# Kernel optimization log

Measured on AMD Instinct MI355X. Metric: run time of the kernel, lower is better.

## Reference

```python
import jax, jax.numpy as jnp
import numpy as np

DIM = 96; NH = 3; HD = DIM // NH; SCALE = HD ** -0.5
WS = (7, 7, 7); N = WS[0] * WS[1] * WS[2]
SHIFT = (3, 3, 3)  # half window
NL = 2
GRID = (28, 28, 28)
B = 2


def _rel_index():
    wd, wh, ww = WS
    coords = np.stack(np.meshgrid(np.arange(wd), np.arange(wh), np.arange(ww), indexing='ij')).reshape(3, -1)
    rel = (coords[:, :, None] - coords[:, None, :]).transpose(1, 2, 0)  # [N,N,3]
    rel[..., 0] += wd - 1; rel[..., 1] += wh - 1; rel[..., 2] += ww - 1
    rel[..., 0] *= (2 * wh - 1) * (2 * ww - 1); rel[..., 1] *= (2 * ww - 1)
    return rel.sum(-1)  # [N,N]

REL_IDX = _rel_index()


def _window_partition(x):
    b, D, H, W, C = x.shape
    wd, wh, ww = WS
    x = x.reshape(b, D // wd, wd, H // wh, wh, W // ww, ww, C)
    x = x.transpose(0, 1, 3, 5, 2, 4, 6, 7)
    return x.reshape(-1, N, C)


def _window_reverse(win, b, D, H, W):
    wd, wh, ww = WS
    C = win.shape[-1]
    x = win.reshape(b, D // wd, H // wh, W // ww, wd, wh, ww, C)
    x = x.transpose(0, 1, 4, 2, 5, 3, 6, 7)
    return x.reshape(b, D, H, W, C)


def _compute_mask():
    # MONAI compute_mask for the shifted (SW-MSA) block
    D, H, W = GRID; wd, wh, ww = WS; sd, sh, sw = SHIFT
    img = np.zeros((1, D, H, W, 1), np.float32)
    cnt = 0
    for d in (slice(-wd), slice(-wd, -sd), slice(-sd, None)):
        for h in (slice(-wh), slice(-wh, -sh), slice(-sh, None)):
            for w in (slice(-ww), slice(-ww, -sw), slice(-sw, None)):
                img[:, d, h, w, :] = cnt; cnt += 1
    mw = img.reshape(1, D // wd, wd, H // wh, wh, W // ww, ww, 1)
    mw = mw.transpose(0, 1, 3, 5, 2, 4, 6, 7).reshape(-1, N)  # [nw, N]
    am = mw[:, None, :] - mw[:, :, None]
    return np.where(am != 0, np.float32(-100.0), np.float32(0.0))

MASK = jnp.asarray(_compute_mask())  # [nw, N, N]


def _ln(x, g, b):
    mu = x.mean(-1, keepdims=True)
    var = ((x - mu) ** 2).mean(-1, keepdims=True)
    return (x - mu) / jnp.sqrt(var + 1e-5) * g + b


def _block(x, p, shift, mask):
    b, D, H, W, C = x.shape
    h = _ln(x, p['n1g'], p['n1b'])
    if shift is not None:
        h = jnp.roll(h, (-shift[0], -shift[1], -shift[2]), axis=(1, 2, 3))
    xw = _window_partition(h)  # [b*nw, N, C]
    Bn = xw.shape[0]
    qkv = (xw @ p['qkvw'].T + p['qkvb']).reshape(Bn, N, 3, NH, HD).transpose(2, 0, 3, 1, 4)
    q, k, v = qkv[0] * SCALE, qkv[1], qkv[2]
    attn = jnp.einsum('bhnd,bhmd->bhnm', q, k)
    bias = p['rel'][REL_IDX.reshape(-1)].reshape(N, N, NH).transpose(2, 0, 1)
    attn = attn + bias[None]
    if mask is not None:
        nw = mask.shape[0]
        attn = (attn.reshape(Bn // nw, nw, NH, N, N) + mask[None, :, None]).reshape(Bn, NH, N, N)
    attn = jax.nn.softmax(attn, axis=-1)
    out = jnp.einsum('bhnm,bhmd->bhnd', attn, v).transpose(0, 2, 1, 3).reshape(Bn, N, C)
    out = out @ p['projw'].T + p['projb']
    h = _window_reverse(out, b, D, H, W)
    if shift is not None:
        h = jnp.roll(h, shift, axis=(1, 2, 3))
    x = x + h
    m = _ln(x, p['n2g'], p['n2b'])
    m = jax.nn.gelu(m @ p['fc1w'].T + p['fc1b'], approximate=False) @ p['fc2w'].T + p['fc2b']
    return x + m


def setup_inputs() -> dict:
    key = jax.random.key(0)
    ks = jax.random.split(key, 8)
    nbias = (2 * WS[0] - 1) * (2 * WS[1] - 1) * (2 * WS[2] - 1)
    return {
        'x': jax.random.normal(ks[0], (B,) + GRID + (DIM,), jnp.float32),
        'norm1_g': jnp.ones((NL, DIM), jnp.float32),
        'norm1_b': jnp.zeros((NL, DIM), jnp.float32),
        'qkv_w': jax.random.normal(ks[1], (NL, 3 * DIM, DIM), jnp.float32) * 0.02,
        'qkv_b': jnp.zeros((NL, 3 * DIM), jnp.float32),
        'rel_bias': jax.random.normal(ks[2], (NL, nbias, NH), jnp.float32) * 0.02,
        'proj_w': jax.random.normal(ks[3], (NL, DIM, DIM), jnp.float32) * 0.02,
        'proj_b': jnp.zeros((NL, DIM), jnp.float32),
        'norm2_g': jnp.ones((NL, DIM), jnp.float32),
        'norm2_b': jnp.zeros((NL, DIM), jnp.float32),
        'fc1_w': jax.random.normal(ks[4], (NL, 4 * DIM, DIM), jnp.float32) * 0.02,
        'fc1_b': jnp.zeros((NL, 4 * DIM), jnp.float32),
        'fc2_w': jax.random.normal(ks[5], (NL, DIM, 4 * DIM), jnp.float32) * 0.02,
        'fc2_b': jnp.zeros((NL, DIM), jnp.float32),
    }


def reference(x, norm1_g, norm1_b, qkv_w, qkv_b, rel_bias, proj_w, proj_b,
              norm2_g, norm2_b, fc1_w, fc1_b, fc2_w, fc2_b):
    for i in range(NL):
        p = dict(n1g=norm1_g[i], n1b=norm1_b[i], qkvw=qkv_w[i], qkvb=qkv_b[i],
                 rel=rel_bias[i], projw=proj_w[i], projb=proj_b[i],
                 n2g=norm2_g[i], n2b=norm2_b[i], fc1w=fc1_w[i], fc1b=fc1_b[i],
                 fc2w=fc2_w[i], fc2b=fc2_b[i])
        if i % 2 == 0:
            x = _block(x, p, None, None)  # W-MSA (mask is all-zero for shift=0)
        else:
            x = _block(x, p, SHIFT, MASK)  # SW-MSA
    return x
```

## Files before the change

### kernel.cpp

```cpp
#include <hip/hip_runtime.h>
#include <math.h>

#define DIM 96
#define NHD 3
#define HD 32
#define NWT 343
#define NWIN 128
#define TOK 43904
#define NBIAS 2197
#define SCALE 0.17677669529663687f
#define TPAD 352

typedef __attribute__((ext_vector_type(8))) short bf16x8;
typedef __attribute__((ext_vector_type(4))) float f32x4;

__device__ __forceinline__ float waveReduceSum(float v) {
    #pragma unroll
    for (int off = 32; off > 0; off >>= 1) v += __shfl_xor(v, off, 64);
    return v;
}

__device__ __forceinline__ unsigned short f2b(float f) {
    union { float f; unsigned int u; } x; x.f = f;
    unsigned int r = (x.u + 0x7fffu + ((x.u >> 16) & 1u)) >> 16;
    return (unsigned short)r;
}
__device__ __forceinline__ unsigned int pk2bf(float a, float b) {
    union { float f; unsigned int u; } x, y; x.f = a; y.f = b;
    return ((x.u + 0x8000u) >> 16) | ((y.u + 0x8000u) & 0xffff0000u);
}

__global__ void __launch_bounds__(256) k_cvt(const float* __restrict__ src,
                                             unsigned short* __restrict__ dst, int n) {
    int i = blockIdx.x * 256 + threadIdx.x;
    if (i < n) dst[i] = f2b(src[i]);
}

__global__ void __launch_bounds__(256) k_ln_part(
        const float* __restrict__ x, const float* __restrict__ g,
        const float* __restrict__ bta, unsigned short* __restrict__ hw, int shift) {
    int wave = (blockIdx.x * blockDim.x + threadIdx.x) >> 6;
    int lane = threadIdx.x & 63;
    if (wave >= TOK) return;
    int bw = wave / NWT, n = wave % NWT;
    int b = bw >> 6, win = bw & 63;
    int wdi = win >> 4, whi = (win >> 2) & 3, wwi = win & 3;
    int d = n / 49, h = (n / 7) % 7, w = n % 7;
    int gd = wdi * 7 + d, gh = whi * 7 + h, gw = wwi * 7 + w;
    int sd = (gd + shift) % 28, sh = (gh + shift) % 28, sw = (gw + shift) % 28;
    const float* row = x + (((size_t)(b * 28 + sd) * 28 + sh) * 28 + sw) * DIM;
    float e0 = row[lane];
    float e1 = (lane < 32) ? row[64 + lane] : 0.0f;
    float s  = waveReduceSum(e0 + e1);
    float mu = s * (1.0f / 96.0f);
    float s2 = waveReduceSum(e0 * e0 + e1 * e1);
    float rstd = rsqrtf(s2 * (1.0f / 96.0f) - mu * mu + 1e-5f);
    unsigned short* dst = hw + (size_t)wave * DIM;
    dst[lane] = f2b((e0 - mu) * rstd * g[lane] + bta[lane]);
    if (lane < 32) dst[64 + lane] = f2b((e1 - mu) * rstd * g[64 + lane] + bta[64 + lane]);
}

__global__ void __launch_bounds__(256) k_qkv(
        const unsigned short* __restrict__ hw, const unsigned short* __restrict__ W,
        const float* __restrict__ bias, unsigned short* __restrict__ q,
        unsigned short* __restrict__ k, unsigned short* __restrict__ v) {
    int wid = threadIdx.x >> 6, lane = threadIdx.x & 63;
    int m0 = blockIdx.x * 64 + wid * 16;
    int lm = lane & 15, q4 = lane >> 4;
    f32x4 acc[18];
    #pragma unroll
    for (int c = 0; c < 18; ++c) acc[c] = (f32x4){0.f, 0.f, 0.f, 0.f};
    const unsigned short* arow = hw + (size_t)(m0 + lm) * 96;
    const unsigned short* brow = W + (size_t)lm * 96;
    #pragma unroll
    for (int ks = 0; ks < 3; ++ks) {
        bf16x8 a = *((const bf16x8*)(arow + ks * 32 + q4 * 8));
        const unsigned short* bp = brow + ks * 32 + q4 * 8;
        #pragma unroll
        for (int c = 0; c < 18; ++c) {
            bf16x8 b = *((const bf16x8*)(bp + c * 16 * 96));
            acc[c] = __builtin_amdgcn_mfma_f32_16x16x32_bf16(a, b, acc[c], 0, 0, 0);
        }
    }
    int bwr[4], nnr[4];
    #pragma unroll
    for (int r = 0; r < 4; ++r) {
        int tok = m0 + q4 * 4 + r;
        bwr[r] = tok / NWT; nnr[r] = tok % NWT;
    }
    #pragma unroll
    for (int c = 0; c < 18; ++c) {
        int n0 = c * 16;
        int which = n0 / 96;
        int col = (n0 % 96) + lm;
        int head = col >> 5, hd = col & 31;
        float bb = bias[n0 + lm];
        #pragma unroll
        for (int r = 0; r < 4; ++r) {
            int wh = bwr[r] * NHD + head;
            float val = acc[c][r] + bb;
            if (which == 0)
                q[(size_t)wh * (TPAD * 32) + nnr[r] * 32 + hd] = f2b(val * SCALE);
            else if (which == 1)
                k[(size_t)wh * (TPAD * 32) + nnr[r] * 32 + hd] = f2b(val);
            else
                v[(size_t)wh * (32 * TPAD) + hd * TPAD + nnr[r]] = f2b(val);
        }
    }
}

__global__ void __launch_bounds__(256) k_attn(
        const unsigned short* __restrict__ q, const unsigned short* __restrict__ k,
        const unsigned short* __restrict__ vT, const float* __restrict__ rel,
        unsigned short* __restrict__ o, int shifted) {
    __shared__ float relh[NBIAS];
    __shared__ int   jinfo[NWT];
    __shared__ __align__(16) unsigned short vts[32 * 360];
    __shared__ __align__(16) unsigned short pbuf[4][16 * 40];
    __shared__ float dnm[4][16];
    int wh = blockIdx.x >> 1, half = blockIdx.x & 1;
    int bw = wh / NHD, head = wh % NHD;
    for (int i = threadIdx.x; i < NBIAS; i += 256) relh[i] = rel[i * NHD + head];
    const unsigned int* vsrc = (const unsigned int*)(vT + (size_t)wh * 32 * TPAD);
    unsigned int* vdst = (unsigned int*)vts;
    for (int i = threadIdx.x; i < 32 * 176; i += 256) {
        int row = i / 176, cc = i - row * 176;
        vdst[row * 180 + cc] = vsrc[i];
    }
    int win = bw & 63;
    int wdi = win >> 4, whi = (win >> 2) & 3, wwi = win & 3;
    for (int i = threadIdx.x; i < NWT; i += 256) {
        int d = i / 49, h = (i / 7) % 7, w = i % 7;
        int gd = wdi * 7 + d, gh = whi * 7 + h, gw = wwi * 7 + w;
        int rd = (gd < 21) ? 0 : ((gd < 25) ? 1 : 2);
        int rh = (gh < 21) ? 0 : ((gh < 25) ? 1 : 2);
        int rw = (gw < 21) ? 0 : ((gw < 25) ? 1 : 2);
        jinfo[i] = (d * 169 + h * 13 + w) | ((rd * 9 + rh * 3 + rw) << 16);
    }
    __syncthreads();
    int wid = threadIdx.x >> 6, lane = threadIdx.x & 63;
    int lm = lane & 15, q4 = lane >> 4;
    const unsigned short* qbase = q + (size_t)wh * TPAD * 32;
    const unsigned short* kbase = k + (size_t)wh * TPAD * 32;
    unsigned short* pb = pbuf[wid];
    for (int qtl = wid; qtl < 11; qtl += 4) {
        int qt = half * 11 + qtl;
        int qtok = qt * 16 + lm;
        bf16x8 qf = *((const bf16x8*)(qbase + qtok * 32 + q4 * 8));
        int jq = jinfo[min(qtok, NWT - 1)];
        int jqc = (jq & 0xffff) + 1098;
        int rq = jq >> 16;
        f32x4 acc0 = (f32x4){0.f, 0.f, 0.f, 0.f};
        f32x4 acc1 = (f32x4){0.f, 0.f, 0.f, 0.f};
        float denom = 0.f;
        for (int pr = 0; pr < 11; ++pr) {
            int kb0 = pr * 32;
            bf16x8 kf0 = *((const bf16x8*)(kbase + (kb0 + lm) * 32 + q4 * 8));
            bf16x8 kf1 = *((const bf16x8*)(kbase + (kb0 + 16 + lm) * 32 + q4 * 8));
            f32x4 z = (f32x4){0.f, 0.f, 0.f, 0.f};
            f32x4 s0 = __builtin_amdgcn_mfma_f32_16x16x32_bf16(kf0, qf, z, 0, 0, 0);
            f32x4 s1 = __builtin_amdgcn_mfma_f32_16x16x32_bf16(kf1, qf, z, 0, 0, 0);
            float p[8];
            #pragma unroll
            for (int t = 0; t < 2; ++t) {
                #pragma unroll
                for (int r = 0; r < 4; ++r) {
                    int key = kb0 + t * 16 + q4 * 4 + r;
                    int jk = jinfo[min(key, NWT - 1)];
                    float s = (t ? s1[r] : s0[r]) + relh[jqc - (jk & 0xffff)];
                    if (shifted && ((jk >> 16) != rq)) s -= 100.0f;
                    float pv = __expf(s);
                    pv = (key < NWT) ? pv : 0.0f;
                    p[t * 4 + r] = pv;
                    denom += pv;
                }
            }
            #pragma unroll
            for (int t = 0; t < 2; ++t) {
                *((unsigned int*)(pb + lm * 40 + t * 16 + q4 * 4)) =
                    pk2bf(p[t * 4 + 0], p[t * 4 + 1]);
                *((unsigned int*)(pb + lm * 40 + t * 16 + q4 * 4 + 2)) =
                    pk2bf(p[t * 4 + 2], p[t * 4 + 3]);
            }
            bf16x8 pf = *((const bf16x8*)(pb + lm * 40 + q4 * 8));
            bf16x8 v0 = *((const bf16x8*)(vts + lm * 360 + kb0 + q4 * 8));
            bf16x8 v1 = *((const bf16x8*)(vts + (16 + lm) * 360 + kb0 + q4 * 8));
            acc0 = __builtin_amdgcn_mfma_f32_16x16x32_bf16(pf, v0, acc0, 0, 0, 0);
            acc1 = __builtin_amdgcn_mfma_f32_16x16x32_bf16(pf, v1, acc1, 0, 0, 0);
        }
        denom += __shfl_xor(denom, 16, 64);
        denom += __shfl_xor(denom, 32, 64);
        if (lane < 16) dnm[wid][lm] = denom;
        #pragma unroll
        for (int r = 0; r < 4; ++r) {
            int qrow = qt * 16 + q4 * 4 + r;
            if (qrow < NWT) {
                float inv = 1.0f / dnm[wid][q4 * 4 + r];
                unsigned short* op = o + (size_t)(bw * NWT + qrow) * DIM + head * HD;
                op[lm]      = f2b(acc0[r] * inv);
                op[16 + lm] = f2b(acc1[r] * inv);
            }
        }
    }
}

__global__ void __launch_bounds__(256) k_proj(
        const unsigned short* __restrict__ ao, const unsigned short* __restrict__ W,
        const float* __restrict__ bias, const float* __restrict__ xin,
        float* __restrict__ xout, unsigned short* __restrict__ lnb,
        const float* __restrict__ g2, const float* __restrict__ b2, int shift) {
    int wid = threadIdx.x >> 6, lane = threadIdx.x & 63;
    int m0 = blockIdx.x * 64 + wid * 16;
    int lm = lane & 15, q4 = lane >> 4;
    f32x4 acc[6];
    #pragma unroll
    for (int c = 0; c < 6; ++c) acc[c] = (f32x4){0.f, 0.f, 0.f, 0.f};
    const unsigned short* arow = ao + (size_t)(m0 + lm) * 96;
    const unsigned short* brow = W + (size_t)lm * 96;
    #pragma unroll
    for (int ks = 0; ks < 3; ++ks) {
        bf16x8 a = *((const bf16x8*)(arow + ks * 32 + q4 * 8));
        const unsigned short* bp = brow + ks * 32 + q4 * 8;
        #pragma unroll
        for (int c = 0; c < 6; ++c) {
            bf16x8 b = *((const bf16x8*)(bp + c * 16 * 96));
            acc[c] = __builtin_amdgcn_mfma_f32_16x16x32_bf16(a, b, acc[c], 0, 0, 0);
        }
    }
    size_t rowoff[4];
    #pragma unroll
    for (int r = 0; r < 4; ++r) {
        int wtok = m0 + q4 * 4 + r;
        int bw = wtok / NWT, n = wtok % NWT;
        int b = bw >> 6, win = bw & 63;
        int wdi = win >> 4, whi = (win >> 2) & 3, wwi = win & 3;
        int d = n / 49, h = (n / 7) % 7, w = n % 7;
        int sd = (wdi * 7 + d + shift) % 28;
        int sh = (whi * 7 + h + shift) % 28;
        int sw = (wwi * 7 + w + shift) % 28;
        rowoff[r] = (((size_t)(b * 28 + sd) * 28 + sh) * 28 + sw) * 96;
    }
    float val[6][4];
    float g2v[6], b2v[6];
    #pragma unroll
    for (int c = 0; c < 6; ++c) {
        int n = c * 16 + lm;
        float bb = bias[n];
        g2v[c] = g2[n]; b2v[c] = b2[n];
        #pragma unroll
        for (int r = 0; r < 4; ++r) {
            size_t off = rowoff[r] + n;
            float y = xin[off] + acc[c][r] + bb;
            val[c][r] = y;
            xout[off] = y;
        }
    }
    #pragma unroll
    for (int r = 0; r < 4; ++r) {
        float s = 0.f, s2 = 0.f;
        #pragma unroll
        for (int c = 0; c < 6; ++c) { s += val[c][r]; s2 += val[c][r] * val[c][r]; }
        #pragma unroll
        for (int off = 8; off > 0; off >>= 1) {
            s  += __shfl_xor(s,  off, 64);
            s2 += __shfl_xor(s2, off, 64);
        }
        float mu = s * (1.0f / 96.0f);
        float rstd = rsqrtf(s2 * (1.0f / 96.0f) - mu * mu + 1e-5f);
        #pragma unroll
        for (int c = 0; c < 6; ++c) {
            lnb[rowoff[r] + c * 16 + lm] =
                f2b((val[c][r] - mu) * rstd * g2v[c] + b2v[c]);
        }
    }
}

__global__ void __launch_bounds__(256) k_mlp(
        const unsigned short* __restrict__ lnb, const float* __restrict__ xmid,
        float* __restrict__ xout,
        const unsigned short* __restrict__ w1, const float* __restrict__ bb1,
        const unsigned short* __restrict__ w2, const float* __restrict__ bb2) {
    __shared__ __align__(16) unsigned short w1s[64][104];
    __shared__ __align__(16) unsigned short w2s[96][76];
    __shared__ __align__(16) unsigned short hid[4][16][76];
    int wid = threadIdx.x >> 6, lane = threadIdx.x & 63;
    int lm = lane & 15, q4 = lane >> 4;
    int m0w = blockIdx.x * 64 + wid * 16;
    bf16x8 a1[3];
    const unsigned short* arow = lnb + (size_t)(m0w + lm) * 96;
    #pragma unroll
    for (int ks = 0; ks < 3; ++ks)
        a1[ks] = *((const bf16x8*)(arow + ks * 32 + q4 * 8));
    f32x4 acc2[6];
    #pragma unroll
    for (int c = 0; c < 6; ++c) acc2[c] = (f32x4){0.f, 0.f, 0.f, 0.f};
    unsigned short* hw_ = &hid[wid][0][0];
    for (int ch = 0; ch < 6; ++ch) {
        __syncthreads();
        const uint4* src1 = (const uint4*)(w1 + ch * 64 * 96);
        #pragma unroll
        for (int t = 0; t < 3; ++t) {
            int s = threadIdx.x + t * 256;
            int row = s / 12, seg = s % 12;
            *((uint4*)&w1s[row][seg * 8]) = src1[s];
        }
        #pragma unroll
        for (int t = 0; t < 3; ++t) {
            int s = threadIdx.x + t * 256;
            int row = s >> 3, seg = s & 7;
            *((uint4*)&w2s[row][seg * 8]) =
                *((const uint4*)(w2 + row * 384 + ch * 64 + seg * 8));
        }
        __syncthreads();
        f32x4 acc1[4];
        #pragma unroll
        for (int t = 0; t < 4; ++t) acc1[t] = (f32x4){0.f, 0.f, 0.f, 0.f};
        #pragma unroll
        for (int ks = 0; ks < 3; ++ks) {
            #pragma unroll
            for (int t = 0; t < 4; ++t) {
                bf16x8 b = *((const bf16x8*)&w1s[t * 16 + lm][ks * 32 + q4 * 8]);
                acc1[t] = __builtin_amdgcn_mfma_f32_16x16x32_bf16(a1[ks], b, acc1[t], 0, 0, 0);
            }
        }
        #pragma unroll
        for (int t = 0; t < 4; ++t) {
            float bb = bb1[ch * 64 + t * 16 + lm];
            #pragma unroll
            for (int r = 0; r < 4; ++r) {
                float v2 = acc1[t][r] + bb;
                float ge = 0.5f * v2 * (1.0f + erff(v2 * 0.70710678118654752f));
                hw_[(q4 * 4 + r) * 76 + t * 16 + lm] = f2b(ge);
            }
        }
        #pragma unroll
        for (int ks2 = 0; ks2 < 2; ++ks2) {
            bf16x8 a = *((const bf16x8*)(hw_ + lm * 76 + ks2 * 32 + q4 * 8));
            #pragma unroll
            for (int c = 0; c < 6; ++c) {
                bf16x8 b = *((const bf16x8*)&w2s[c * 16 + lm][ks2 * 32 + q4 * 8]);
                acc2[c] = __builtin_amdgcn_mfma_f32_16x16x32_bf16(a, b, acc2[c], 0, 0, 0);
            }
        }
    }
    #pragma unroll
    for (int c = 0; c < 6; ++c) {
        int n = c * 16 + lm;
        float bb = bb2[n];
        #pragma unroll
        for (int r = 0; r < 4; ++r) {
            size_t off = (size_t)(m0w + q4 * 4 + r) * 96 + n;
            xout[off] = xmid[off] + acc2[c][r] + bb;
        }
    }
}

extern "C" void kernel_launch(void* const* d_in, const int* in_sizes, int n_in,
                              void* d_out, int out_size, void* d_ws, size_t ws_size,
                              hipStream_t stream) {
    const float* x     = (const float*)d_in[0];
    const float* n1g   = (const float*)d_in[1];
    const float* n1b   = (const float*)d_in[2];
    const float* qkvw  = (const float*)d_in[3];
    const float* qkvb  = (const float*)d_in[4];
    const float* relb  = (const float*)d_in[5];
    const float* projw = (const float*)d_in[6];
    const float* projb = (const float*)d_in[7];
    const float* n2g   = (const float*)d_in[8];
    const float* n2b   = (const float*)d_in[9];
    const float* fc1w  = (const float*)d_in[10];
    const float* fc1b  = (const float*)d_in[11];
    const float* fc2w  = (const float*)d_in[12];
    const float* fc2b  = (const float*)d_in[13];
    float* out = (float*)d_out;

    const size_t NEL = (size_t)TOK * DIM;
    const size_t QKN = (size_t)NWIN * NHD * TPAD * 32;
    float* buf_x = (float*)d_ws;
    unsigned short* hbuf = (unsigned short*)(buf_x + NEL);
    unsigned short* lnb  = hbuf + NEL;
    unsigned short* bq   = lnb + NEL;
    unsigned short* bk   = bq + QKN;
    unsigned short* bv   = bk + QKN;
    unsigned short* wts  = bv + QKN;
    unsigned short* wq  = wts;
    unsigned short* wp  = wq + 2 * 27648;
    unsigned short* w1  = wp + 2 * 9216;
    unsigned short* w2  = w1 + 2 * 36864;

    k_cvt<<<(2 * 27648 + 255) / 256, 256, 0, stream>>>(qkvw, wq, 2 * 27648);
    k_cvt<<<(2 * 9216  + 255) / 256, 256, 0, stream>>>(projw, wp, 2 * 9216);
    k_cvt<<<(2 * 36864 + 255) / 256, 256, 0, stream>>>(fc1w, w1, 2 * 36864);
    k_cvt<<<(2 * 36864 + 255) / 256, 256, 0, stream>>>(fc2w, w2, 2 * 36864);

    for (int L = 0; L < 2; ++L) {
        int shift = (L == 0) ? 0 : 3;
        const float* xin_l = (L == 0) ? x : buf_x;
        float* xmid = buf_x;
        float* xfin = (L == 0) ? buf_x : out;

        k_ln_part<<<TOK / 4, 256, 0, stream>>>(xin_l, n1g + L * 96, n1b + L * 96, hbuf, shift);
        k_qkv<<<TOK / 64, 256, 0, stream>>>(hbuf, wq + L * 27648, qkvb + L * 288, bq, bk, bv);
        k_attn<<<NWIN * NHD * 2, 256, 0, stream>>>(bq, bk, bv, relb + L * NBIAS * NHD, hbuf,
                                                   shift ? 1 : 0);
        k_proj<<<TOK / 64, 256, 0, stream>>>(hbuf, wp + L * 9216, projb + L * 96,
                                             xin_l, buf_x, lnb,
                                             n2g + L * 96, n2b + L * 96, shift);
        k_mlp<<<TOK / 64, 256, 0, stream>>>(lnb, buf_x, xfin,
                                            w1 + L * 36864, fc1b + L * 384,
                                            w2 + L * 36864, fc2b + L * 96);
    }
}
```

Baseline: 325.5 us.

## Fuse LayerNorm1 and shifted gather into QKV GEMM, stage weights in LDS

Removes the separate LN+window-partition kernel. The QKV kernel now reads fp32 rows directly with the roll/partition index math, normalizes them, and writes bf16 into LDS as the MFMA A operand. This eliminates a bf16 intermediate write and read plus one launch per layer. QKV weights are now staged into padded LDS in three chunks, and the proj kernel also stages its weights in LDS, replacing repeated global loads of B fragments. The cost is extra syncthreads and LDS traffic per block.

```diff
diff --git a/kernel.cpp b/kernel.cpp
--- a/kernel.cpp
+++ b/kernel.cpp
@@ -14,12 +14,6 @@
 typedef __attribute__((ext_vector_type(8))) short bf16x8;
 typedef __attribute__((ext_vector_type(4))) float f32x4;
 
-__device__ __forceinline__ float waveReduceSum(float v) {
-    #pragma unroll
-    for (int off = 32; off > 0; off >>= 1) v += __shfl_xor(v, off, 64);
-    return v;
-}
-
 __device__ __forceinline__ unsigned short f2b(float f) {
     union { float f; unsigned int u; } x; x.f = f;
     unsigned int r = (x.u + 0x7fffu + ((x.u >> 16) & 1u)) >> 16;
@@ -36,75 +30,96 @@
     if (i < n) dst[i] = f2b(src[i]);
 }
 
-__global__ void __launch_bounds__(256) k_ln_part(
-        const float* __restrict__ x, const float* __restrict__ g,
-        const float* __restrict__ bta, unsigned short* __restrict__ hw, int shift) {
-    int wave = (blockIdx.x * blockDim.x + threadIdx.x) >> 6;
-    int lane = threadIdx.x & 63;
-    if (wave >= TOK) return;
-    int bw = wave / NWT, n = wave % NWT;
-    int b = bw >> 6, win = bw & 63;
-    int wdi = win >> 4, whi = (win >> 2) & 3, wwi = win & 3;
-    int d = n / 49, h = (n / 7) % 7, w = n % 7;
-    int gd = wdi * 7 + d, gh = whi * 7 + h, gw = wwi * 7 + w;
-    int sd = (gd + shift) % 28, sh = (gh + shift) % 28, sw = (gw + shift) % 28;
-    const float* row = x + (((size_t)(b * 28 + sd) * 28 + sh) * 28 + sw) * DIM;
-    float e0 = row[lane];
-    float e1 = (lane < 32) ? row[64 + lane] : 0.0f;
-    float s  = waveReduceSum(e0 + e1);
-    float mu = s * (1.0f / 96.0f);
-    float s2 = waveReduceSum(e0 * e0 + e1 * e1);
-    float rstd = rsqrtf(s2 * (1.0f / 96.0f) - mu * mu + 1e-5f);
-    unsigned short* dst = hw + (size_t)wave * DIM;
-    dst[lane] = f2b((e0 - mu) * rstd * g[lane] + bta[lane]);
-    if (lane < 32) dst[64 + lane] = f2b((e1 - mu) * rstd * g[64 + lane] + bta[64 + lane]);
-}
-
 __global__ void __launch_bounds__(256) k_qkv(
-        const unsigned short* __restrict__ hw, const unsigned short* __restrict__ W,
+        const float* __restrict__ x, const float* __restrict__ g1,
+        const float* __restrict__ b1, const unsigned short* __restrict__ W,
         const float* __restrict__ bias, unsigned short* __restrict__ q,
-        unsigned short* __restrict__ k, unsigned short* __restrict__ v) {
+        unsigned short* __restrict__ k, unsigned short* __restrict__ v, int shift) {
+    __shared__ __align__(16) unsigned short lns[64][104];
+    __shared__ __align__(16) unsigned short wbuf[96][104];
     int wid = threadIdx.x >> 6, lane = threadIdx.x & 63;
+    int lm = lane & 15, q4 = lane >> 4;
     int m0 = blockIdx.x * 64 + wid * 16;
-    int lm = lane & 15, q4 = lane >> 4;
-    f32x4 acc[18];
-    #pragma unroll
-    for (int c = 0; c < 18; ++c) acc[c] = (f32x4){0.f, 0.f, 0.f, 0.f};
-    const unsigned short* arow = hw + (size_t)(m0 + lm) * 96;
-    const unsigned short* brow = W + (size_t)lm * 96;
-    #pragma unroll
-    for (int ks = 0; ks < 3; ++ks) {
-        bf16x8 a = *((const bf16x8*)(arow + ks * 32 + q4 * 8));
-        const unsigned short* bp = brow + ks * 32 + q4 * 8;
-        #pragma unroll
-        for (int c = 0; c < 18; ++c) {
-            bf16x8 b = *((const bf16x8*)(bp + c * 16 * 96));
-            acc[c] = __builtin_amdgcn_mfma_f32_16x16x32_bf16(a, b, acc[c], 0, 0, 0);
-        }
-    }
     int bwr[4], nnr[4];
+    size_t rowoff[4];
     #pragma unroll
     for (int r = 0; r < 4; ++r) {
-        int tok = m0 + q4 * 4 + r;
-        bwr[r] = tok / NWT; nnr[r] = tok % NWT;
-    }
-    #pragma unroll
-    for (int c = 0; c < 18; ++c) {
-        int n0 = c * 16;
-        int which = n0 / 96;
-        int col = (n0 % 96) + lm;
-        int head = col >> 5, hd = col & 31;
-        float bb = bias[n0 + lm];
-        #pragma unroll
-        for (int r = 0; r < 4; ++r) {
-            int wh = bwr[r] * NHD + head;
-            float val = acc[c][r] + bb;
-            if (which == 0)
-                q[(size_t)wh * (TPAD * 32) + nnr[r] * 32 + hd] = f2b(val * SCALE);
-            else if (which == 1)
-                k[(size_t)wh * (TPAD * 32) + nnr[r] * 32 + hd] = f2b(val);
-            else
-                v[(size_t)wh * (32 * TPAD) + hd * TPAD + nnr[r]] = f2b(val);
+        int wtok = m0 + q4 * 4 + r;
+        int bw = wtok / NWT, n = wtok % NWT;
+        bwr[r] = bw; nnr[r] = n;
+        int b = bw >> 6, win = bw & 63;
+        int wdi = win >> 4, whi = (win >> 2) & 3, wwi = win & 3;
+        int d = n / 49, h = (n / 7) % 7, w = n % 7;
+        int sd = (wdi * 7 + d + shift) % 28;
+        int sh = (whi * 7 + h + shift) % 28;
+        int sw = (wwi * 7 + w + shift) % 28;
+        rowoff[r] = (((size_t)(b * 28 + sd) * 28 + sh) * 28 + sw) * 96;
+    }
+    float val[6][4], g1v[6], b1v[6];
+    #pragma unroll
+    for (int c = 0; c < 6; ++c) {
+        int ncol = c * 16 + lm;
+        g1v[c] = g1[ncol]; b1v[c] = b1[ncol];
+        #pragma unroll
+        for (int r = 0; r < 4; ++r) val[c][r] = x[rowoff[r] + ncol];
+    }
+    #pragma unroll
+    for (int r = 0; r < 4; ++r) {
+        float s = 0.f, s2 = 0.f;
+        #pragma unroll
+        for (int c = 0; c < 6; ++c) { s += val[c][r]; s2 += val[c][r] * val[c][r]; }
+        #pragma unroll
+        for (int off = 8; off > 0; off >>= 1) {
+            s  += __shfl_xor(s,  off, 64);
+            s2 += __shfl_xor(s2, off, 64);
+        }
+        float mu = s * (1.0f / 96.0f);
+        float rstd = rsqrtf(s2 * (1.0f / 96.0f) - mu * mu + 1e-5f);
+        int row = wid * 16 + q4 * 4 + r;
+        #pragma unroll
+        for (int c = 0; c < 6; ++c)
+            lns[row][c * 16 + lm] = f2b((val[c][r] - mu) * rstd * g1v[c] + b1v[c]);
+    }
+    __syncthreads();
+    bf16x8 a1[3];
+    #pragma unroll
+    for (int ks = 0; ks < 3; ++ks)
+        a1[ks] = *((const bf16x8*)&lns[wid * 16 + lm][ks * 32 + q4 * 8]);
+    for (int ch = 0; ch < 3; ++ch) {
+        __syncthreads();
+        const uint4* src = (const uint4*)(W + ch * 96 * 96);
+        for (int s = threadIdx.x; s < 1152; s += 256) {
+            int row = s / 12, seg = s % 12;
+            *((uint4*)&wbuf[row][seg * 8]) = src[s];
+        }
+        __syncthreads();
+        f32x4 acc[6];
+        #pragma unroll
+        for (int c = 0; c < 6; ++c) acc[c] = (f32x4){0.f, 0.f, 0.f, 0.f};
+        #pragma unroll
+        for (int ks = 0; ks < 3; ++ks) {
+            #pragma unroll
+            for (int c = 0; c < 6; ++c) {
+                bf16x8 b = *((const bf16x8*)&wbuf[c * 16 + lm][ks * 32 + q4 * 8]);
+                acc[c] = __builtin_amdgcn_mfma_f32_16x16x32_bf16(a1[ks], b, acc[c], 0, 0, 0);
+            }
+        }
+        #pragma unroll
+        for (int c = 0; c < 6; ++c) {
+            int col = c * 16 + lm;
+            int head = col >> 5, hd = col & 31;
+            float bb = bias[ch * 96 + col];
+            #pragma unroll
+            for (int r = 0; r < 4; ++r) {
+                int wh = bwr[r] * NHD + head;
+                float vv = acc[c][r] + bb;
+                if (ch == 0)
+                    q[(size_t)wh * (TPAD * 32) + nnr[r] * 32 + hd] = f2b(vv * SCALE);
+                else if (ch == 1)
+                    k[(size_t)wh * (TPAD * 32) + nnr[r] * 32 + hd] = f2b(vv);
+                else
+                    v[(size_t)wh * (32 * TPAD) + hd * TPAD + nnr[r]] = f2b(vv);
+            }
         }
     }
 }
@@ -209,22 +224,29 @@
         const float* __restrict__ bias, const float* __restrict__ xin,
         float* __restrict__ xout, unsigned short* __restrict__ lnb,
         const float* __restrict__ g2, const float* __restrict__ b2, int shift) {
+    __shared__ __align__(16) unsigned short wbuf[96][104];
+    for (int s = threadIdx.x; s < 1152; s += 256) {
+        int row = s / 12, seg = s % 12;
+        *((uint4*)&wbuf[row][seg * 8]) = ((const uint4*)W)[s];
+    }
     int wid = threadIdx.x >> 6, lane = threadIdx.x & 63;
     int m0 = blockIdx.x * 64 + wid * 16;
     int lm = lane & 15, q4 = lane >> 4;
+    const unsigned short* arow = ao + (size_t)(m0 + lm) * 96;
+    bf16x8 a1[3];
+    #pragma unroll
+    for (int ks = 0; ks < 3; ++ks)
+        a1[ks] = *((const bf16x8*)(arow + ks * 32 + q4 * 8));
+    __syncthreads();
     f32x4 acc[6];
     #pragma unroll
     for (int c = 0; c < 6; ++c) acc[c] = (f32x4){0.f, 0.f, 0.f, 0.f};
-    const unsigned short* arow = ao + (size_t)(m0 + lm) * 96;
-    const unsigned short* brow = W + (size_t)lm * 96;
     #pragma unroll
     for (int ks = 0; ks < 3; ++ks) {
-        bf16x8 a = *((const bf16x8*)(arow + ks * 32 + q4 * 8));
-        const unsigned short* bp = brow + ks * 32 + q4 * 8;
         #pragma unroll
         for (int c = 0; c < 6; ++c) {
-            bf16x8 b = *((const bf16x8*)(bp + c * 16 * 96));
-            acc[c] = __builtin_amdgcn_mfma_f32_16x16x32_bf16(a, b, acc[c], 0, 0, 0);
+            bf16x8 b = *((const bf16x8*)&wbuf[c * 16 + lm][ks * 32 + q4 * 8]);
+            acc[c] = __builtin_amdgcn_mfma_f32_16x16x32_bf16(a1[ks], b, acc[c], 0, 0, 0);
         }
     }
     size_t rowoff[4];
@@ -396,11 +418,11 @@
     for (int L = 0; L < 2; ++L) {
         int shift = (L == 0) ? 0 : 3;
         const float* xin_l = (L == 0) ? x : buf_x;
-        float* xmid = buf_x;
         float* xfin = (L == 0) ? buf_x : out;
 
-        k_ln_part<<<TOK / 4, 256, 0, stream>>>(xin_l, n1g + L * 96, n1b + L * 96, hbuf, shift);
-        k_qkv<<<TOK / 64, 256, 0, stream>>>(hbuf, wq + L * 27648, qkvb + L * 288, bq, bk, bv);
+        k_qkv<<<TOK / 64, 256, 0, stream>>>(xin_l, n1g + L * 96, n1b + L * 96,
+                                            wq + L * 27648, qkvb + L * 288,
+                                            bq, bk, bv, shift);
         k_attn<<<NWIN * NHD * 2, 256, 0, stream>>>(bq, bk, bv, relb + L * NBIAS * NHD, hbuf,
                                                    shift ? 1 : 0);
         k_proj<<<TOK / 64, 256, 0, stream>>>(hbuf, wp + L * 9216, projb + L * 96,
```

Result: faster. 295.5 us (-9.2%).
